# Kernel optimization log

Hardware: AMD Instinct MI355X
Metric: run time of the kernel (lower is better)

## Reference

```python
import jax, jax.numpy as jnp
import numpy as np

DIM = 256      # model/channel dim (== dim_inner)
DT_RANK = 16   # low-rank dt projection
D_STATE = 16   # SSM state size N
BATCH = 4
SEQLEN = 4096


def setup_inputs() -> dict:
    key = jax.random.key(0)
    ks = jax.random.split(key, 8)
    s = 1.0 / np.sqrt(DIM)
    x = jax.random.normal(ks[0], (BATCH, SEQLEN, DIM), jnp.float32)
    W_proj = jax.random.normal(ks[1], (DIM, DIM), jnp.float32) * s
    b_proj = jax.random.normal(ks[2], (DIM,), jnp.float32) * s
    conv_w = jax.random.normal(ks[3], (DIM, 3), jnp.float32) * 0.3   # depthwise kernel, taps [t-1, t, t+1]
    conv_b = jnp.zeros((DIM,), jnp.float32)
    W_dbc = jax.random.normal(ks[4], (DIM, DT_RANK + 2 * D_STATE), jnp.float32) * s  # -> [delta_lowrank | B | C]
    W_dt = jax.random.normal(ks[5], (DT_RANK, DIM), jnp.float32) / np.sqrt(DT_RANK)
    b_dt = jax.random.normal(ks[6], (DIM,), jnp.float32) * 0.1
    A_log = jnp.log(jnp.broadcast_to(jnp.arange(1, D_STATE + 1, dtype=jnp.float32), (DIM, D_STATE)))
    D_skip = jnp.ones((DIM,), jnp.float32)
    return dict(x=x, W_proj=W_proj, b_proj=b_proj, conv_w=conv_w, conv_b=conv_b,
                W_dbc=W_dbc, W_dt=W_dt, b_dt=b_dt, A_log=A_log, D_skip=D_skip)


def reference(x, W_proj, b_proj, conv_w, conv_b, W_dbc, W_dt, b_dt, A_log, D_skip):
    skip = x
    x_one = x @ W_proj + b_proj            # (B,L,D)
    x_two = x @ W_proj + b_proj            # same (single) linear, per the module's prof/proj
    # depthwise Conv1d(kernel=3, padding=1, groups=D) over the sequence axis
    xp = jnp.pad(x_one, ((0, 0), (1, 1), (0, 0)))
    x_one = (xp[:, :-2] * conv_w[:, 0] + xp[:, 1:-1] * conv_w[:, 1]
             + xp[:, 2:] * conv_w[:, 2]) + conv_b
    x_one = jax.nn.silu(x_one)
    # --- selective-scan SSM ---
    A = -jnp.exp(A_log)                    # (D,N)
    dbc = x_one @ W_dbc                    # (B,L,DT+2N)
    delta, Bm, Cm = jnp.split(dbc, [DT_RANK, DT_RANK + D_STATE], axis=-1)
    delta = jax.nn.softplus(delta @ W_dt + b_dt)                 # (B,L,D)
    deltaA = jnp.exp(delta[..., None] * A)                       # (B,L,D,N)
    deltaBX = delta[..., None] * Bm[:, :, None, :] * x_one[..., None]  # (B,L,D,N)

    def step(h, ab):
        a_t, b_t = ab
        h = a_t * h + b_t
        return h, h

    h0 = jnp.zeros((x.shape[0], DIM, D_STATE), x.dtype)
    _, hs = jax.lax.scan(step, h0, (deltaA.swapaxes(0, 1), deltaBX.swapaxes(0, 1)))
    hs = hs.swapaxes(0, 1)                                       # (B,L,D,N)
    y = jnp.einsum('bldn,bln->bld', hs, Cm) + D_skip * x_one     # SSM output
    # gated residual
    out = y * jax.nn.silu(x_two) + skip
    return out @ W_proj + b_proj
```

## Files before the change

kernel.cpp:

```cpp
#include <hip/hip_runtime.h>
#include <math.h>

#define B_ 4
#define L_ 4096
#define D_ 256
#define N_ 16
#define DTR 16
#define NC 128
#define LC 32
#define M_ (B_*L_)

typedef __attribute__((ext_vector_type(8))) short short8;
typedef __attribute__((ext_vector_type(4))) float floatx4;

__device__ __forceinline__ float silu_f(float v) { return v / (1.f + __expf(-v)); }

__device__ __forceinline__ unsigned short f2bf(float f) {
  union { float f; unsigned u; } v; v.f = f;
  unsigned r = (v.u + 0x7FFFu + ((v.u >> 16) & 1u)) >> 16;
  return (unsigned short)r;
}
__device__ __forceinline__ float bf2f(unsigned short s) {
  union { unsigned u; float f; } v; v.u = (unsigned)s << 16; return v.f;
}
__device__ __forceinline__ float bflo(unsigned u) {
  union { unsigned u; float f; } v; v.u = u << 16; return v.f;
}
__device__ __forceinline__ float bfhi(unsigned u) {
  union { unsigned u; float f; } v; v.u = u & 0xFFFF0000u; return v.f;
}

__device__ __forceinline__ float softplus_f(float x) {
  return fmaxf(x, 0.f) + __logf(1.f + __expf(-fabsf(x)));
}

__global__ __launch_bounds__(256) void convert_w_k(
    const float* __restrict__ W, const float* __restrict__ Wdbc,
    unsigned short* __restrict__ Wt, unsigned short* __restrict__ Wdbct)
{
  const int k = blockIdx.x;
  const int n = threadIdx.x;
  Wt[n * 256 + k] = f2bf(W[k * 256 + n]);
  if (n < 48) Wdbct[n * 256 + k] = f2bf(Wdbc[k * 48 + n]);
}

__global__ __launch_bounds__(512) void gemm_mfma_k(
    const float* __restrict__ Asrc, const unsigned short* __restrict__ Wt,
    const float* __restrict__ bias, float* __restrict__ Cout)
{
  __shared__ unsigned short Asl[32][40];
  __shared__ unsigned short Wsl[256][40];
  const int tid = threadIdx.x;
  const int lane = tid & 63, w = tid >> 6;
  const int row0 = blockIdx.x * 32;
  const int l15 = lane & 15, lg = lane >> 4;
  const int arow = (w & 1) * 16 + l15;
  const int ctile = (w >> 1) * 64;
  const int kk = lg * 8;
  floatx4 acc[4];
  #pragma unroll
  for (int f = 0; f < 4; ++f) acc[f] = (floatx4){0.f, 0.f, 0.f, 0.f};

  const int ar = tid >> 4, akc = (tid & 15) * 2;
  const int wn = tid >> 1, wkc = (tid & 1) * 16;

  for (int ks = 0; ks < 8; ++ks) {
    const int k0 = ks * 32;
    __syncthreads();
    {
      const int off = (row0 + ar) * 256 + k0 + akc;
      const float2 av = *(const float2*)(Asrc + off);
      unsigned short* p = &Asl[ar][akc];
      p[0] = f2bf(av.x); p[1] = f2bf(av.y);
    }
    *(uint4*)&Wsl[wn][wkc + 0] = *(const uint4*)(Wt + wn * 256 + k0 + wkc);
    *(uint4*)&Wsl[wn][wkc + 8] = *(const uint4*)(Wt + wn * 256 + k0 + wkc + 8);
    __syncthreads();
    const short8 af = *(const short8*)&Asl[arow][kk];
    #pragma unroll
    for (int f = 0; f < 4; ++f) {
      const short8 bf_ = *(const short8*)&Wsl[ctile + f * 16 + l15][kk];
      acc[f] = __builtin_amdgcn_mfma_f32_16x16x32_bf16(af, bf_, acc[f], 0, 0, 0);
    }
  }
  const int growb = row0 + (w & 1) * 16 + lg * 4;
  #pragma unroll
  for (int f = 0; f < 4; ++f) {
    const int col = ctile + f * 16 + l15;
    const float bb = bias[col];
    #pragma unroll
    for (int r = 0; r < 4; ++r)
      Cout[(growb + r) * 256 + col] = acc[f][r] + bb;
  }
}

__global__ __launch_bounds__(512) void conv_dbc_delta_scan1_k(
    const float* __restrict__ lin, const float* __restrict__ conv_w,
    const float* __restrict__ conv_b, const unsigned short* __restrict__ Wdbct,
    const float* __restrict__ Wdt, const float* __restrict__ bdt,
    const float* __restrict__ A_log,
    unsigned* __restrict__ dxc,
    float* __restrict__ Bm, float* __restrict__ Cm,
    float* __restrict__ Pp, float* __restrict__ Sp)
{
  __shared__ unsigned short xcb[32][264];
  __shared__ unsigned short dlt[32][264];
  __shared__ float dlow[32][17];
  __shared__ float Bsh[32][17];
  const int blk = blockIdx.x;
  const int b  = blk >> 7;
  const int c  = blk & (NC - 1);
  const int l0 = c * LC;
  const int tid = threadIdx.x;
  const int lane = tid & 63, w = tid >> 6;
  const int l15 = lane & 15, lg = lane >> 4;

  for (int q = tid; q < 32 * 64; q += 512) {
    const int r = q >> 6, dq = (q & 63) * 4;
    const int l = l0 + r;
    const int base = (b * L_ + l) * D_ + dq;
    float4 c0 = (l > 0)      ? *(const float4*)(lin + base - D_) : make_float4(0,0,0,0);
    float4 c1 = *(const float4*)(lin + base);
    float4 c2 = (l < L_ - 1) ? *(const float4*)(lin + base + D_) : make_float4(0,0,0,0);
    float4 v;
    v.x = silu_f(c0.x*conv_w[(dq+0)*3+0] + c1.x*conv_w[(dq+0)*3+1] + c2.x*conv_w[(dq+0)*3+2] + conv_b[dq+0]);
    v.y = silu_f(c0.y*conv_w[(dq+1)*3+0] + c1.y*conv_w[(dq+1)*3+1] + c2.y*conv_w[(dq+1)*3+2] + conv_b[dq+1]);
    v.z = silu_f(c0.z*conv_w[(dq+2)*3+0] + c1.z*conv_w[(dq+2)*3+1] + c2.z*conv_w[(dq+2)*3+2] + conv_b[dq+2]);
    v.w = silu_f(c0.w*conv_w[(dq+3)*3+0] + c1.w*conv_w[(dq+3)*3+1] + c2.w*conv_w[(dq+3)*3+2] + conv_b[dq+3]);
    ushort4 bv;
    bv.x = f2bf(v.x); bv.y = f2bf(v.y); bv.z = f2bf(v.z); bv.w = f2bf(v.w);
    *(ushort4*)&xcb[r][dq] = bv;
  }
  __syncthreads();

  if (w < 2) {
    const int arow = w * 16 + l15;
    const int kk0 = lg * 8;
    floatx4 acc[3];
    #pragma unroll
    for (int nt = 0; nt < 3; ++nt) acc[nt] = (floatx4){0.f, 0.f, 0.f, 0.f};
    #pragma unroll
    for (int ks = 0; ks < 8; ++ks) {
      const short8 af = *(const short8*)&xcb[arow][ks * 32 + kk0];
      #pragma unroll
      for (int nt = 0; nt < 3; ++nt) {
        const short8 bf_ = *(const short8*)(Wdbct + (nt * 16 + l15) * 256 + ks * 32 + kk0);
        acc[nt] = __builtin_amdgcn_mfma_f32_16x16x32_bf16(af, bf_, acc[nt], 0, 0, 0);
      }
    }
    const int row = w * 16 + lg * 4;
    const int gl = (b * L_ + l0 + row) * N_ + l15;
    #pragma unroll
    for (int r = 0; r < 4; ++r) {
      dlow[row + r][l15]   = acc[0][r];
      Bsh[row + r][l15]    = acc[1][r];
      Bm[gl + r * N_]      = acc[1][r];
      Cm[gl + r * N_]      = acc[2][r];
    }
  }
  __syncthreads();

  for (int q = tid; q < 32 * 64; q += 512) {
    const int r = q >> 6, dq = (q & 63) * 4;
    float4 s = *(const float4*)(bdt + dq);
    #pragma unroll
    for (int k = 0; k < DTR; ++k) {
      const float f = dlow[r][k];
      const float4 wv = *(const float4*)(Wdt + k * D_ + dq);
      s.x = fmaf(f, wv.x, s.x); s.y = fmaf(f, wv.y, s.y);
      s.z = fmaf(f, wv.z, s.z); s.w = fmaf(f, wv.w, s.w);
    }
    ushort4 dv;
    dv.x = f2bf(softplus_f(s.x)); dv.y = f2bf(softplus_f(s.y));
    dv.z = f2bf(softplus_f(s.z)); dv.w = f2bf(softplus_f(s.w));
    *(ushort4*)&dlt[r][dq] = dv;
    uint4 o;
    o.x = (unsigned)dv.x | ((unsigned)xcb[r][dq + 0] << 16);
    o.y = (unsigned)dv.y | ((unsigned)xcb[r][dq + 1] << 16);
    o.z = (unsigned)dv.z | ((unsigned)xcb[r][dq + 2] << 16);
    o.w = (unsigned)dv.w | ((unsigned)xcb[r][dq + 3] << 16);
    *(uint4*)(dxc + (b * L_ + (l0 + r)) * D_ + dq) = o;
  }
  __syncthreads();

  {
    const int nh = tid & 1, d = tid >> 1, n0 = nh * 8;
    float A[8], P[8], S[8];
    bool fast = true;
    #pragma unroll
    for (int n = 0; n < 8; ++n) {
      A[n] = -__expf(A_log[d * N_ + n0 + n]);
      const float k = (float)(n0 + n + 1);
      fast = fast && (fabsf(A[n] + k) < 1e-3f * k);
      P[n] = 1.f; S[n] = 0.f;
    }
    if (fast) {
      float sumdv = 0.f;
      for (int t = 0; t < LC; ++t) {
        const float dv = bf2f(dlt[t][d]);
        const float xv = bf2f(xcb[t][d]);
        const float dvx = dv * xv;
        const float rr = __expf(-dv);
        sumdv += dv;
        float a;
        if (nh) { const float r2 = rr * rr, r4 = r2 * r2; a = r4 * r4 * rr; }
        else    a = rr;
        #pragma unroll
        for (int n = 0; n < 8; ++n) {
          S[n] = fmaf(a, S[n], dvx * Bsh[t][n0 + n]);
          a *= rr;
        }
      }
      const float R = __expf(-sumdv);
      float pr;
      if (nh) { const float R2 = R * R, R4 = R2 * R2; pr = R4 * R4 * R; }
      else    pr = R;
      #pragma unroll
      for (int n = 0; n < 8; ++n) { P[n] = pr; pr *= R; }
    } else {
      for (int t = 0; t < LC; ++t) {
        const float dv = bf2f(dlt[t][d]);
        const float xv = bf2f(xcb[t][d]);
        const float dvx = dv * xv;
        #pragma unroll
        for (int n = 0; n < 8; ++n) {
          const float a = __expf(dv * A[n]);
          S[n] = fmaf(a, S[n], dvx * Bsh[t][n0 + n]);
          P[n] *= a;
        }
      }
    }
    const int o = ((b * D_ + d) * NC + c) * N_ + n0;
    *(float4*)(Pp + o)     = *(const float4*)&P[0];
    *(float4*)(Pp + o + 4) = *(const float4*)&P[4];
    *(float4*)(Sp + o)     = *(const float4*)&S[0];
    *(float4*)(Sp + o + 4) = *(const float4*)&S[4];
  }
}

__global__ __launch_bounds__(128) void scan_pass2_k(
    const float* Pp, const float* Sp, float* Hin)
{
  __shared__ float lP[N_][NC + 1];
  __shared__ float lS[N_][NC + 1];
  const int bd = blockIdx.x;
  const int c = threadIdx.x;
  const int base = bd * NC * N_ + c * N_;
  float P[N_], S[N_];
  #pragma unroll
  for (int q = 0; q < 4; ++q) {
    *(float4*)&P[q * 4] = *(const float4*)(Pp + base + q * 4);
    *(float4*)&S[q * 4] = *(const float4*)(Sp + base + q * 4);
  }
  #pragma unroll
  for (int n = 0; n < N_; ++n) { lP[n][c] = P[n]; lS[n][c] = S[n]; }
  for (int s = 1; s < NC; s <<= 1) {
    __syncthreads();
    float Pb[N_], Sb[N_];
    if (c >= s) {
      #pragma unroll
      for (int n = 0; n < N_; ++n) { Pb[n] = lP[n][c - s]; Sb[n] = lS[n][c - s]; }
    }
    __syncthreads();
    if (c >= s) {
      #pragma unroll
      for (int n = 0; n < N_; ++n) {
        S[n] = fmaf(P[n], Sb[n], S[n]);
        P[n] *= Pb[n];
        lP[n][c] = P[n]; lS[n][c] = S[n];
      }
    }
  }
  __syncthreads();
  float h[N_];
  if (c == 0) {
    #pragma unroll
    for (int n = 0; n < N_; ++n) h[n] = 0.f;
  } else {
    #pragma unroll
    for (int n = 0; n < N_; ++n) h[n] = lS[n][c - 1];
  }
  #pragma unroll
  for (int q = 0; q < 4; ++q)
    *(float4*)(Hin + base + q * 4) = *(const float4*)&h[q * 4];
}

__global__ __launch_bounds__(512) void scan3_gemm2_k(
    const unsigned* __restrict__ dxc,
    const float* __restrict__ Bm, const float* __restrict__ Cm,
    const float* __restrict__ A_log, const float* __restrict__ Dskip,
    const float* __restrict__ Hin, const float* __restrict__ lin,
    const float* __restrict__ xin, const unsigned short* __restrict__ Wt,
    const float* __restrict__ bias, float* __restrict__ out)
{
  __shared__ unsigned short Asl[32][264];
  __shared__ unsigned short Wsl[256][40];
  __shared__ float Bs[LC][N_];
  __shared__ float Cs[LC][N_];
  const int blk = blockIdx.x;
  const int b = blk >> 7, c = blk & (NC - 1);
  const int tid = threadIdx.x;
  const int row0 = blk * 32;

  {
    const int src = (b * L_ + c * LC) * N_ + tid;
    Bs[tid >> 4][tid & 15] = Bm[src];
    Cs[tid >> 4][tid & 15] = Cm[src];
  }
  __syncthreads();

  {
    const int nh = tid & 1, d = tid >> 1, n0 = nh * 8;
    const float dsk = Dskip[d];
    float A[8], h[8];
    bool fast = true;
    const int ho = ((b * D_ + d) * NC + c) * N_ + n0;
    #pragma unroll
    for (int n = 0; n < 8; ++n) {
      A[n] = -__expf(A_log[d * N_ + n0 + n]);
      const float k = (float)(n0 + n + 1);
      fast = fast && (fabsf(A[n] + k) < 1e-3f * k);
    }
    *(float4*)&h[0] = *(const float4*)(Hin + ho);
    *(float4*)&h[4] = *(const float4*)(Hin + ho + 4);
    int base = (b * L_ + c * LC) * D_ + d;
    unsigned u = dxc[base];
    if (fast) {
      #pragma unroll 4
      for (int t = 0; t < LC; ++t) {
        const unsigned u_n = (t < LC - 1) ? dxc[base + D_] : 0u;
        const float dv = bflo(u), xv = bfhi(u);
        const float dvx = dv * xv;
        float bv[8], cv[8];
        *(float4*)&bv[0] = *(const float4*)&Bs[t][n0];
        *(float4*)&bv[4] = *(const float4*)&Bs[t][n0 + 4];
        *(float4*)&cv[0] = *(const float4*)&Cs[t][n0];
        *(float4*)&cv[4] = *(const float4*)&Cs[t][n0 + 4];
        const float r = __expf(-dv);
        float a;
        if (nh) { const float r2 = r * r, r4 = r2 * r2; a = r4 * r4 * r; }
        else    a = r;
        float p = 0.f;
        #pragma unroll
        for (int n = 0; n < 8; ++n) {
          h[n] = fmaf(a, h[n], dvx * bv[n]);
          p = fmaf(h[n], cv[n], p);
          a *= r;
        }
        p += __shfl_xor(p, 1);
        if (nh == 0) Asl[t][d] = f2bf(fmaf(dsk, xv, p));
        u = u_n; base += D_;
      }
    } else {
      for (int t = 0; t < LC; ++t) {
        const unsigned uu = dxc[base];
        const float dvv = bflo(uu);
        const float xvv = bfhi(uu);
        const float dvx = dvv * xvv;
        float bv[8], cv[8];
        *(float4*)&bv[0] = *(const float4*)&Bs[t][n0];
        *(float4*)&bv[4] = *(const float4*)&Bs[t][n0 + 4];
        *(float4*)&cv[0] = *(const float4*)&Cs[t][n0];
        *(float4*)&cv[4] = *(const float4*)&Cs[t][n0 + 4];
        float p = 0.f;
        #pragma unroll
        for (int n = 0; n < 8; ++n) {
          const float a = __expf(dvv * A[n]);
          h[n] = fmaf(a, h[n], dvx * bv[n]);
          p = fmaf(h[n], cv[n], p);
        }
        p += __shfl_xor(p, 1);
        if (nh == 0) Asl[t][d] = f2bf(fmaf(dsk, xvv, p));
        base += D_;
      }
    }
  }
  __syncthreads();

  for (int q = tid; q < 32 * 64; q += 512) {
    const int r = q >> 6, dq = (q & 63) * 4;
    const int off = (row0 + r) * 256 + dq;
    const float4 lv = *(const float4*)(lin + off);
    const float4 xv = *(const float4*)(xin + off);
    ushort4 yv = *(const ushort4*)&Asl[r][dq];
    ushort4 av;
    av.x = f2bf(fmaf(bf2f(yv.x), silu_f(lv.x), xv.x));
    av.y = f2bf(fmaf(bf2f(yv.y), silu_f(lv.y), xv.y));
    av.z = f2bf(fmaf(bf2f(yv.z), silu_f(lv.z), xv.z));
    av.w = f2bf(fmaf(bf2f(yv.w), silu_f(lv.w), xv.w));
    *(ushort4*)&Asl[r][dq] = av;
  }

  const int lane = tid & 63, w = tid >> 6;
  const int l15 = lane & 15, lg = lane >> 4;
  const int arow = (w & 1) * 16 + l15;
  const int ctile = (w >> 1) * 64;
  const int kk = lg * 8;
  const int wn = tid >> 1, wkc = (tid & 1) * 16;
  floatx4 acc[4];
  #pragma unroll
  for (int f = 0; f < 4; ++f) acc[f] = (floatx4){0.f, 0.f, 0.f, 0.f};

  for (int ks = 0; ks < 8; ++ks) {
    __syncthreads();
    *(uint4*)&Wsl[wn][wkc + 0] = *(const uint4*)(Wt + wn * 256 + ks * 32 + wkc);
    *(uint4*)&Wsl[wn][wkc + 8] = *(const uint4*)(Wt + wn * 256 + ks * 32 + wkc + 8);
    __syncthreads();
    const short8 af = *(const short8*)&Asl[arow][ks * 32 + kk];
    #pragma unroll
    for (int f = 0; f < 4; ++f) {
      const short8 bf_ = *(const short8*)&Wsl[ctile + f * 16 + l15][kk];
      acc[f] = __builtin_amdgcn_mfma_f32_16x16x32_bf16(af, bf_, acc[f], 0, 0, 0);
    }
  }
  const int growb = row0 + (w & 1) * 16 + lg * 4;
  #pragma unroll
  for (int f = 0; f < 4; ++f) {
    const int col = ctile + f * 16 + l15;
    const float bb = bias[col];
    #pragma unroll
    for (int r = 0; r < 4; ++r)
      out[(growb + r) * 256 + col] = acc[f][r] + bb;
  }
}

extern "C" void kernel_launch(void* const* d_in, const int* in_sizes, int n_in,
                              void* d_out, int out_size, void* d_ws, size_t ws_size,
                              hipStream_t stream) {
  const float* x      = (const float*)d_in[0];
  const float* W_proj = (const float*)d_in[1];
  const float* b_proj = (const float*)d_in[2];
  const float* conv_w = (const float*)d_in[3];
  const float* conv_b = (const float*)d_in[4];
  const float* W_dbc  = (const float*)d_in[5];
  const float* W_dt   = (const float*)d_in[6];
  const float* b_dt   = (const float*)d_in[7];
  const float* A_log  = (const float*)d_in[8];
  const float* D_skip = (const float*)d_in[9];
  float* out = (float*)d_out;

  float* ws    = (float*)d_ws;
  const size_t SZ = (size_t)M_ * D_;
  const size_t PSZ = (size_t)B_ * D_ * NC * N_;
  float*    lin = ws;
  unsigned* dxc = (unsigned*)(ws + SZ);
  float*    Pp  = ws + 2 * SZ;
  float*    Sp  = Pp + PSZ;
  float*    Hin = Pp;
  float*    Bm  = ws + 3 * SZ;
  float*    Cm  = Bm + (size_t)M_ * N_;
  unsigned short* Wt    = (unsigned short*)(Cm + (size_t)M_ * N_);
  unsigned short* Wdbct = Wt + 256 * 256;

  convert_w_k<<<dim3(256), dim3(256), 0, stream>>>(W_proj, W_dbc, Wt, Wdbct);
  gemm_mfma_k<<<dim3(512), dim3(512), 0, stream>>>(x, Wt, b_proj, lin);
  conv_dbc_delta_scan1_k<<<dim3(512), dim3(512), 0, stream>>>(
      lin, conv_w, conv_b, Wdbct, W_dt, b_dt, A_log, dxc, Bm, Cm, Pp, Sp);
  scan_pass2_k<<<dim3(1024), dim3(128), 0, stream>>>(Pp, Sp, Hin);
  scan3_gemm2_k<<<dim3(512), dim3(512), 0, stream>>>(
      dxc, Bm, Cm, A_log, D_skip, Hin, lin, x, Wt, b_proj, out);
}
```

Baseline: 81.13 us.

## Fuse input projection GEMM into conv/scan kernel and store projection as bf16

Removes the standalone projection GEMM kernel. Each conv block now recomputes the x@W_proj tile for its 32 rows plus halo rows (48 rows total) directly in LDS with MFMA, then applies the depthwise conv from shared memory. The projection output needed later for the gate is written as bf16 instead of fp32, which halves that traffic. The cost is about 50% redundant GEMM work on the halo rows, more LDS use per block, and lower precision on the gate input.

```diff
diff --git a/kernel.cpp b/kernel.cpp
--- a/kernel.cpp
+++ b/kernel.cpp
@@ -44,69 +44,24 @@
   if (n < 48) Wdbct[n * 256 + k] = f2bf(Wdbc[k * 48 + n]);
 }
 
-__global__ __launch_bounds__(512) void gemm_mfma_k(
-    const float* __restrict__ Asrc, const unsigned short* __restrict__ Wt,
-    const float* __restrict__ bias, float* __restrict__ Cout)
-{
-  __shared__ unsigned short Asl[32][40];
-  __shared__ unsigned short Wsl[256][40];
-  const int tid = threadIdx.x;
-  const int lane = tid & 63, w = tid >> 6;
-  const int row0 = blockIdx.x * 32;
-  const int l15 = lane & 15, lg = lane >> 4;
-  const int arow = (w & 1) * 16 + l15;
-  const int ctile = (w >> 1) * 64;
-  const int kk = lg * 8;
-  floatx4 acc[4];
-  #pragma unroll
-  for (int f = 0; f < 4; ++f) acc[f] = (floatx4){0.f, 0.f, 0.f, 0.f};
-
-  const int ar = tid >> 4, akc = (tid & 15) * 2;
-  const int wn = tid >> 1, wkc = (tid & 1) * 16;
-
-  for (int ks = 0; ks < 8; ++ks) {
-    const int k0 = ks * 32;
-    __syncthreads();
-    {
-      const int off = (row0 + ar) * 256 + k0 + akc;
-      const float2 av = *(const float2*)(Asrc + off);
-      unsigned short* p = &Asl[ar][akc];
-      p[0] = f2bf(av.x); p[1] = f2bf(av.y);
-    }
-    *(uint4*)&Wsl[wn][wkc + 0] = *(const uint4*)(Wt + wn * 256 + k0 + wkc);
-    *(uint4*)&Wsl[wn][wkc + 8] = *(const uint4*)(Wt + wn * 256 + k0 + wkc + 8);
-    __syncthreads();
-    const short8 af = *(const short8*)&Asl[arow][kk];
-    #pragma unroll
-    for (int f = 0; f < 4; ++f) {
-      const short8 bf_ = *(const short8*)&Wsl[ctile + f * 16 + l15][kk];
-      acc[f] = __builtin_amdgcn_mfma_f32_16x16x32_bf16(af, bf_, acc[f], 0, 0, 0);
-    }
-  }
-  const int growb = row0 + (w & 1) * 16 + lg * 4;
-  #pragma unroll
-  for (int f = 0; f < 4; ++f) {
-    const int col = ctile + f * 16 + l15;
-    const float bb = bias[col];
-    #pragma unroll
-    for (int r = 0; r < 4; ++r)
-      Cout[(growb + r) * 256 + col] = acc[f][r] + bb;
-  }
-}
-
-__global__ __launch_bounds__(512) void conv_dbc_delta_scan1_k(
-    const float* __restrict__ lin, const float* __restrict__ conv_w,
-    const float* __restrict__ conv_b, const unsigned short* __restrict__ Wdbct,
+__global__ __launch_bounds__(512) void conv_all_k(
+    const float* __restrict__ x, const float* __restrict__ conv_w,
+    const float* __restrict__ conv_b, const unsigned short* __restrict__ Wt,
+    const unsigned short* __restrict__ Wdbct,
     const float* __restrict__ Wdt, const float* __restrict__ bdt,
-    const float* __restrict__ A_log,
-    unsigned* __restrict__ dxc,
+    const float* __restrict__ A_log, const float* __restrict__ bias,
+    unsigned short* __restrict__ lin16, unsigned* __restrict__ dxc,
     float* __restrict__ Bm, float* __restrict__ Cm,
     float* __restrict__ Pp, float* __restrict__ Sp)
 {
+  __shared__ __align__(16) char smA[25344];
+  __shared__ unsigned short linb[48][264];
   __shared__ unsigned short xcb[32][264];
-  __shared__ unsigned short dlt[32][264];
-  __shared__ float dlow[32][17];
-  __shared__ float Bsh[32][17];
+  unsigned short (*xsa)[264] = (unsigned short(*)[264])smA;
+  unsigned short (*dlt)[264] = (unsigned short(*)[264])smA;
+  float (*dlow)[17] = (float(*)[17])(smA + 16896);
+  float (*Bsh)[17]  = (float(*)[17])(smA + 16896 + 2176);
+
   const int blk = blockIdx.x;
   const int b  = blk >> 7;
   const int c  = blk & (NC - 1);
@@ -114,19 +69,67 @@
   const int tid = threadIdx.x;
   const int lane = tid & 63, w = tid >> 6;
   const int l15 = lane & 15, lg = lane >> 4;
+  const int kk = lg * 8;
+
+  for (int q = tid; q < 48 * 64; q += 512) {
+    const int row = q >> 6, f4 = (q & 63) * 4;
+    int g = b * L_ + l0 - 8 + row;
+    g = g < 0 ? 0 : (g >= M_ ? M_ - 1 : g);
+    const float4 v = *(const float4*)(x + (size_t)g * 256 + f4);
+    ushort4 bv;
+    bv.x = f2bf(v.x); bv.y = f2bf(v.y); bv.z = f2bf(v.z); bv.w = f2bf(v.w);
+    *(ushort4*)&xsa[row][f4] = bv;
+  }
+  __syncthreads();
+
+  {
+    const int c0w = w * 32;
+    floatx4 acc[3][2];
+    #pragma unroll
+    for (int rg = 0; rg < 3; ++rg)
+      #pragma unroll
+      for (int f = 0; f < 2; ++f) acc[rg][f] = (floatx4){0.f, 0.f, 0.f, 0.f};
+    #pragma unroll
+    for (int ks = 0; ks < 8; ++ks) {
+      const short8 af0 = *(const short8*)&xsa[ 0 + l15][ks * 32 + kk];
+      const short8 af1 = *(const short8*)&xsa[16 + l15][ks * 32 + kk];
+      const short8 af2 = *(const short8*)&xsa[32 + l15][ks * 32 + kk];
+      #pragma unroll
+      for (int f = 0; f < 2; ++f) {
+        const short8 bf_ = *(const short8*)(Wt + (c0w + f * 16 + l15) * 256 + ks * 32 + kk);
+        acc[0][f] = __builtin_amdgcn_mfma_f32_16x16x32_bf16(af0, bf_, acc[0][f], 0, 0, 0);
+        acc[1][f] = __builtin_amdgcn_mfma_f32_16x16x32_bf16(af1, bf_, acc[1][f], 0, 0, 0);
+        acc[2][f] = __builtin_amdgcn_mfma_f32_16x16x32_bf16(af2, bf_, acc[2][f], 0, 0, 0);
+      }
+    }
+    __syncthreads();
+    #pragma unroll
+    for (int rg = 0; rg < 3; ++rg)
+      #pragma unroll
+      for (int f = 0; f < 2; ++f) {
+        const int col = c0w + f * 16 + l15;
+        const float bb = bias[col];
+        #pragma unroll
+        for (int r = 0; r < 4; ++r)
+          linb[rg * 16 + lg * 4 + r][col] = f2bf(acc[rg][f][r] + bb);
+      }
+  }
+  __syncthreads();
 
   for (int q = tid; q < 32 * 64; q += 512) {
     const int r = q >> 6, dq = (q & 63) * 4;
     const int l = l0 + r;
-    const int base = (b * L_ + l) * D_ + dq;
-    float4 c0 = (l > 0)      ? *(const float4*)(lin + base - D_) : make_float4(0,0,0,0);
-    float4 c1 = *(const float4*)(lin + base);
-    float4 c2 = (l < L_ - 1) ? *(const float4*)(lin + base + D_) : make_float4(0,0,0,0);
+    const int lr = r + 8;
+    const ushort4 z = {0, 0, 0, 0};
+    const ushort4 c0u = (l > 0)      ? *(const ushort4*)&linb[lr - 1][dq] : z;
+    const ushort4 c1u = *(const ushort4*)&linb[lr][dq];
+    const ushort4 c2u = (l < L_ - 1) ? *(const ushort4*)&linb[lr + 1][dq] : z;
+    *(ushort4*)(lin16 + (size_t)(b * L_ + l) * D_ + dq) = c1u;
     float4 v;
-    v.x = silu_f(c0.x*conv_w[(dq+0)*3+0] + c1.x*conv_w[(dq+0)*3+1] + c2.x*conv_w[(dq+0)*3+2] + conv_b[dq+0]);
-    v.y = silu_f(c0.y*conv_w[(dq+1)*3+0] + c1.y*conv_w[(dq+1)*3+1] + c2.y*conv_w[(dq+1)*3+2] + conv_b[dq+1]);
-    v.z = silu_f(c0.z*conv_w[(dq+2)*3+0] + c1.z*conv_w[(dq+2)*3+1] + c2.z*conv_w[(dq+2)*3+2] + conv_b[dq+2]);
-    v.w = silu_f(c0.w*conv_w[(dq+3)*3+0] + c1.w*conv_w[(dq+3)*3+1] + c2.w*conv_w[(dq+3)*3+2] + conv_b[dq+3]);
+    v.x = silu_f(bf2f(c0u.x)*conv_w[(dq+0)*3+0] + bf2f(c1u.x)*conv_w[(dq+0)*3+1] + bf2f(c2u.x)*conv_w[(dq+0)*3+2] + conv_b[dq+0]);
+    v.y = silu_f(bf2f(c0u.y)*conv_w[(dq+1)*3+0] + bf2f(c1u.y)*conv_w[(dq+1)*3+1] + bf2f(c2u.y)*conv_w[(dq+1)*3+2] + conv_b[dq+1]);
+    v.z = silu_f(bf2f(c0u.z)*conv_w[(dq+2)*3+0] + bf2f(c1u.z)*conv_w[(dq+2)*3+1] + bf2f(c2u.z)*conv_w[(dq+2)*3+2] + conv_b[dq+2]);
+    v.w = silu_f(bf2f(c0u.w)*conv_w[(dq+3)*3+0] + bf2f(c1u.w)*conv_w[(dq+3)*3+1] + bf2f(c2u.w)*conv_w[(dq+3)*3+2] + conv_b[dq+3]);
     ushort4 bv;
     bv.x = f2bf(v.x); bv.y = f2bf(v.y); bv.z = f2bf(v.z); bv.w = f2bf(v.w);
     *(ushort4*)&xcb[r][dq] = bv;
@@ -135,16 +138,15 @@
 
   if (w < 2) {
     const int arow = w * 16 + l15;
-    const int kk0 = lg * 8;
     floatx4 acc[3];
     #pragma unroll
     for (int nt = 0; nt < 3; ++nt) acc[nt] = (floatx4){0.f, 0.f, 0.f, 0.f};
     #pragma unroll
     for (int ks = 0; ks < 8; ++ks) {
-      const short8 af = *(const short8*)&xcb[arow][ks * 32 + kk0];
+      const short8 af = *(const short8*)&xcb[arow][ks * 32 + kk];
       #pragma unroll
       for (int nt = 0; nt < 3; ++nt) {
-        const short8 bf_ = *(const short8*)(Wdbct + (nt * 16 + l15) * 256 + ks * 32 + kk0);
+        const short8 bf_ = *(const short8*)(Wdbct + (nt * 16 + l15) * 256 + ks * 32 + kk);
         acc[nt] = __builtin_amdgcn_mfma_f32_16x16x32_bf16(af, bf_, acc[nt], 0, 0, 0);
       }
     }
@@ -179,7 +181,7 @@
     o.y = (unsigned)dv.y | ((unsigned)xcb[r][dq + 1] << 16);
     o.z = (unsigned)dv.z | ((unsigned)xcb[r][dq + 2] << 16);
     o.w = (unsigned)dv.w | ((unsigned)xcb[r][dq + 3] << 16);
-    *(uint4*)(dxc + (b * L_ + (l0 + r)) * D_ + dq) = o;
+    *(uint4*)(dxc + (size_t)(b * L_ + (l0 + r)) * D_ + dq) = o;
   }
   __syncthreads();
 
@@ -289,7 +291,7 @@
     const unsigned* __restrict__ dxc,
     const float* __restrict__ Bm, const float* __restrict__ Cm,
     const float* __restrict__ A_log, const float* __restrict__ Dskip,
-    const float* __restrict__ Hin, const float* __restrict__ lin,
+    const float* __restrict__ Hin, const unsigned short* __restrict__ lin16,
     const float* __restrict__ xin, const unsigned short* __restrict__ Wt,
     const float* __restrict__ bias, float* __restrict__ out)
 {
@@ -380,14 +382,14 @@
   for (int q = tid; q < 32 * 64; q += 512) {
     const int r = q >> 6, dq = (q & 63) * 4;
     const int off = (row0 + r) * 256 + dq;
-    const float4 lv = *(const float4*)(lin + off);
-    const float4 xv = *(const float4*)(xin + off);
+    const ushort4 lv = *(const ushort4*)(lin16 + off);
+    const float4  xv = *(const float4*)(xin + off);
     ushort4 yv = *(const ushort4*)&Asl[r][dq];
     ushort4 av;
-    av.x = f2bf(fmaf(bf2f(yv.x), silu_f(lv.x), xv.x));
-    av.y = f2bf(fmaf(bf2f(yv.y), silu_f(lv.y), xv.y));
-    av.z = f2bf(fmaf(bf2f(yv.z), silu_f(lv.z), xv.z));
-    av.w = f2bf(fmaf(bf2f(yv.w), silu_f(lv.w), xv.w));
+    av.x = f2bf(fmaf(bf2f(yv.x), silu_f(bf2f(lv.x)), xv.x));
+    av.y = f2bf(fmaf(bf2f(yv.y), silu_f(bf2f(lv.y)), xv.y));
+    av.z = f2bf(fmaf(bf2f(yv.z), silu_f(bf2f(lv.z)), xv.z));
+    av.w = f2bf(fmaf(bf2f(yv.w), silu_f(bf2f(lv.w)), xv.w));
     *(ushort4*)&Asl[r][dq] = av;
   }
 
@@ -442,7 +444,7 @@
   float* ws    = (float*)d_ws;
   const size_t SZ = (size_t)M_ * D_;
   const size_t PSZ = (size_t)B_ * D_ * NC * N_;
-  float*    lin = ws;
+  unsigned short* lin16 = (unsigned short*)ws;
   unsigned* dxc = (unsigned*)(ws + SZ);
   float*    Pp  = ws + 2 * SZ;
   float*    Sp  = Pp + PSZ;
@@ -453,10 +455,10 @@
   unsigned short* Wdbct = Wt + 256 * 256;
 
   convert_w_k<<<dim3(256), dim3(256), 0, stream>>>(W_proj, W_dbc, Wt, Wdbct);
-  gemm_mfma_k<<<dim3(512), dim3(512), 0, stream>>>(x, Wt, b_proj, lin);
-  conv_dbc_delta_scan1_k<<<dim3(512), dim3(512), 0, stream>>>(
-      lin, conv_w, conv_b, Wdbct, W_dt, b_dt, A_log, dxc, Bm, Cm, Pp, Sp);
+  conv_all_k<<<dim3(512), dim3(512), 0, stream>>>(
+      x, conv_w, conv_b, Wt, Wdbct, W_dt, b_dt, A_log, b_proj,
+      lin16, dxc, Bm, Cm, Pp, Sp);
   scan_pass2_k<<<dim3(1024), dim3(128), 0, stream>>>(Pp, Sp, Hin);
   scan3_gemm2_k<<<dim3(512), dim3(512), 0, stream>>>(
-      dxc, Bm, Cm, A_log, D_skip, Hin, lin, x, Wt, b_proj, out);
-}
+      dxc, Bm, Cm, A_log, D_skip, Hin, lin16, x, Wt, b_proj, out);
+}
```

Measured after the change: 78.54 us, median of 3. 1.03x faster.
